# Optimization experiments

Hardware: AMD Instinct MI355X
Metric: run time of the kernel (lower is better)

Reference implementation:

```python
import jax, jax.numpy as jnp
import numpy as np

N_NODES = 50000
N_EDGES = 800000
D_IN = 128
D_OUT = 128
D_RED = 32  # out_features // reduction
ORDER = 3


def setup_inputs() -> dict:
    key = jax.random.key(0)
    ks = jax.random.split(key, 16)
    s = 1.0 / np.sqrt(D_IN)
    inp = {
        'features': jax.random.normal(ks[0], (N_NODES, D_IN), jnp.float32),
        'edge_row': jax.random.randint(ks[1], (N_EDGES,), 0, N_NODES, jnp.int32),
        'edge_col': jax.random.randint(ks[2], (N_EDGES,), 0, N_NODES, jnp.int32),
        'edge_val': jax.random.uniform(ks[3], (N_EDGES,), jnp.float32) / 16.0,  # ~1/avg_degree normalization
        'w1': jax.random.normal(ks[4], (D_IN, D_OUT), jnp.float32) * s,
        'b1': jax.random.normal(ks[5], (D_OUT,), jnp.float32) * s,
        'w2': jax.random.normal(ks[6], (D_IN, D_OUT), jnp.float32) * s,
        'b2': jax.random.normal(ks[7], (D_OUT,), jnp.float32) * s,
        'w3': jax.random.normal(ks[8], (D_IN, D_OUT), jnp.float32) * s,
        'b3': jax.random.normal(ks[9], (D_OUT,), jnp.float32) * s,
        'fc1_w': jax.random.normal(ks[10], (D_OUT, D_RED), jnp.float32) * s,
        'fc1_b': jax.random.normal(ks[11], (D_RED,), jnp.float32) * s,
        'fc2_w': jax.random.normal(ks[12], (D_RED, D_OUT), jnp.float32) * (1.0 / np.sqrt(D_RED)),
        'fc2_b': jax.random.normal(ks[13], (D_OUT,), jnp.float32) * s,
    }
    return inp


def reference(features, edge_row, edge_col, edge_val, w1, b1, w2, b2, w3, b3,
              fc1_w, fc1_b, fc2_w, fc2_b):
    def spmm(x):  # sparse [N,N] @ dense [N,D] via gather + segment_sum
        msgs = edge_val[:, None] * x[edge_col]          # [E, D]
        return jax.ops.segment_sum(msgs, edge_row, num_segments=N_NODES)

    def ngnn(w, b, order):
        h = jnp.tanh(features @ w)                      # active=True path
        for _ in range(order):                          # order spmm hops
            h = spmm(h)
        return h + b

    abstract = [ngnn(w, b, k + 1) for k, (w, b) in enumerate([(w1, b1), (w2, b2), (w3, b3)])]
    feats = jnp.stack(abstract, axis=0)                 # [order, N, D]
    m = jnp.mean(feats, axis=1)                         # [order, D]
    a = jax.nn.relu(m @ fc1_w + fc1_b) @ fc2_w + fc2_b  # [order, D]
    a = jax.nn.softmax(a, axis=0)                       # softmax over order dim
    out = jnp.einsum('ond,od->nd', feats, a)            # weighted combine
    return out
```

## Files before the change

### kernel.cpp

```cpp
#include <hip/hip_runtime.h>
#include <cstdint>

#define N_NODES 50000
#define N_EDGES 800000
#define EPCAP 64

typedef _Float16 half8 __attribute__((ext_vector_type(8)));
typedef float f32x4 __attribute__((ext_vector_type(4)));


__device__ inline unsigned pack_half2(float lo, float hi) {
    union { _Float16 h[2]; unsigned u; } cv;
    cv.h[0] = (_Float16)lo; cv.h[1] = (_Float16)hi;
    return cv.u;
}
__device__ inline float h_lo(unsigned u) {
    union { unsigned u; _Float16 h[2]; } cv; cv.u = u; return (float)cv.h[0];
}
__device__ inline float h_hi(unsigned u) {
    union { unsigned u; _Float16 h[2]; } cv; cv.u = u; return (float)cv.h[1];
}


__global__ __launch_bounds__(256) void pre_kernel(const int* __restrict__ rows,
                                                  const int* __restrict__ cols,
                                                  const float* __restrict__ vals,
                                                  int* __restrict__ cnt,
                                                  unsigned* __restrict__ ep,
                                                  const float* __restrict__ F,
                                                  const float* __restrict__ w3,
                                                  const float* __restrict__ w2,
                                                  const float* __restrict__ w1,
                                                  unsigned* __restrict__ T1) {
    __shared__ _Float16 Ws[128 * 128];
    int bx = blockIdx.x;
    int tid = threadIdx.x;

    if (bx >= 782) {
        int e = (bx - 782) * 256 + tid;
        int r = rows[e];
        int p = atomicAdd(&cnt[r], 1);
        union { _Float16 h; unsigned short s; } cv; cv.h = (_Float16)vals[e];
        if (p < EPCAP)
            __builtin_nontemporal_store(((unsigned)cv.s << 16) | (unsigned)cols[e],
                                        &ep[(size_t)r * EPCAP + p]);
        return;
    }

    int lane = tid & 63, wv = tid >> 6;
    int c = lane & 15, g = lane >> 4;
    int rowbase = bx * 64;

    half8 afr[4];
    {
        int row = rowbase + wv * 16 + c;
        if (row >= N_NODES) row = N_NODES - 1;
        const float* fr = F + (size_t)row * 128;
        #pragma unroll
        for (int ks = 0; ks < 4; ++ks) {
            const float4* s4 = (const float4*)(fr + ks * 32 + g * 8);
            float4 x0 = s4[0], x1 = s4[1];
            half8 a;
            a[0] = (_Float16)x0.x; a[1] = (_Float16)x0.y;
            a[2] = (_Float16)x0.z; a[3] = (_Float16)x0.w;
            a[4] = (_Float16)x1.x; a[5] = (_Float16)x1.y;
            a[6] = (_Float16)x1.z; a[7] = (_Float16)x1.w;
            afr[ks] = a;
        }
    }

    for (int b = 0; b < 3; ++b) {
        const float* W = (b == 0) ? w3 : (b == 1) ? w2 : w1;
        for (int i = tid; i < 16384; i += 256) {
            int d = i >> 7, j = i & 127;
            *(_Float16*)((char*)Ws + (((j * 128 + d) * 2) ^ ((j & 15) << 4))) = (_Float16)W[i];
        }
        __syncthreads();

        f32x4 zero = {0.f, 0.f, 0.f, 0.f};
        f32x4 acc[8];
        #pragma unroll
        for (int t = 0; t < 8; ++t) acc[t] = zero;

        #pragma unroll
        for (int ks = 0; ks < 4; ++ks) {
            #pragma unroll
            for (int t = 0; t < 8; ++t) {
                int j = t * 16 + c;
                int off = ((j * 128 + ks * 32 + g * 8) * 2) ^ ((j & 15) << 4);
                half8 bfr = *(const half8*)((const char*)Ws + off);
                acc[t] = __builtin_amdgcn_mfma_f32_16x16x32_f16(afr[ks], bfr, acc[t], 0, 0, 0);
            }
        }

        #pragma unroll
        for (int t = 0; t < 4; ++t) {
            int j = t * 16 + c;
            #pragma unroll
            for (int r = 0; r < 4; ++r) {
                int row = rowbase + wv * 16 + g * 4 + r;
                if (row < N_NODES)
                    T1[(size_t)row * 192 + b * 64 + j] =
                        pack_half2(tanhf(acc[t][r]), tanhf(acc[t + 4][r]));
            }
        }
        __syncthreads();
    }
}


template <int NCHUNK>
__global__ __launch_bounds__(512) void spmm_stage_kernel(const int* __restrict__ cnts,
                                                         const unsigned* __restrict__ ep,
                                                         const unsigned* __restrict__ x,
                                                         unsigned* __restrict__ ob0,
                                                         unsigned* __restrict__ obf,
                                                         float* __restrict__ csumK) {
    __shared__ float cs[128];
    int tid = threadIdx.x;
    if (tid < 128) cs[tid] = 0.f;
    __syncthreads();

    int row = blockIdx.x * 8 + (tid >> 6);
    int lane = tid & 63;
    int n = __builtin_amdgcn_readfirstlane(cnts[row]);
    n = n < EPCAP ? n : EPCAP;
    const unsigned* e0 = ep + (size_t)row * EPCAP;

    float ax[NCHUNK], ay[NCHUNK];
    #pragma unroll
    for (int cc = 0; cc < NCHUNK; ++cc) { ax[cc] = 0.f; ay[cc] = 0.f; }

    const unsigned* xl = x + lane;
    constexpr int U = 8;
    int i = 0;
    for (; i + U <= n; i += U) {
        unsigned p[U];
        #pragma unroll
        for (int u = 0; u < U; ++u) p[u] = e0[i + u];
        unsigned gx[U][NCHUNK];
        #pragma unroll
        for (int u = 0; u < U; ++u) {
            unsigned b = (p[u] & 0xFFFFu) * (unsigned)(NCHUNK * 64);
            #pragma unroll
            for (int cc = 0; cc < NCHUNK; ++cc) gx[u][cc] = xl[b + cc * 64];
        }
        #pragma unroll
        for (int u = 0; u < U; ++u) {
            union { unsigned short s; _Float16 h; } cu; cu.s = (unsigned short)(p[u] >> 16);
            float v = (float)cu.h;
            #pragma unroll
            for (int cc = 0; cc < NCHUNK; ++cc) {
                ax[cc] += v * h_lo(gx[u][cc]);
                ay[cc] += v * h_hi(gx[u][cc]);
            }
        }
    }
    for (; i < n; ++i) {
        unsigned p = e0[i];
        unsigned b = (p & 0xFFFFu) * (unsigned)(NCHUNK * 64);
        union { unsigned short s; _Float16 h; } cu; cu.s = (unsigned short)(p >> 16);
        float v = (float)cu.h;
        #pragma unroll
        for (int cc = 0; cc < NCHUNK; ++cc) {
            unsigned gg = xl[b + cc * 64];
            ax[cc] += v * h_lo(gg);
            ay[cc] += v * h_hi(gg);
        }
    }

    #pragma unroll
    for (int cc = 0; cc < NCHUNK - 1; ++cc)
        ob0[(size_t)row * ((NCHUNK - 1) * 64) + cc * 64 + lane] = pack_half2(ax[cc], ay[cc]);

    float fx = ax[NCHUNK - 1], fy = ay[NCHUNK - 1];
    obf[(size_t)row * 64 + lane] = pack_half2(fx, fy);
    atomicAdd(&cs[2 * lane + 0], fx);
    atomicAdd(&cs[2 * lane + 1], fy);
    __syncthreads();
    if (tid < 128) atomicAdd(&csumK[(blockIdx.x & 7) * 384 + tid], cs[tid]);
}


__global__ __launch_bounds__(256) void combine_kernel(float* __restrict__ out,
                                                      const unsigned* __restrict__ f1,
                                                      const unsigned* __restrict__ f2,
                                                      const unsigned* __restrict__ f3,
                                                      const float* __restrict__ csum,
                                                      const float* __restrict__ b1,
                                                      const float* __restrict__ b2,
                                                      const float* __restrict__ b3,
                                                      const float* __restrict__ fc1w,
                                                      const float* __restrict__ fc1b,
                                                      const float* __restrict__ fc2w,
                                                      const float* __restrict__ fc2b) {
    __shared__ float m[3][128];
    __shared__ float rr[3][32];
    __shared__ float wgt[3][128];
    int t = threadIdx.x;

    if (t < 128) {
        const float inv = 1.0f / (float)N_NODES;
        int slot = (t < 64) ? (2 * t) : (2 * (t - 64) + 1);
        #pragma unroll
        for (int k = 0; k < 3; ++k) {
            float s = 0.f;
            #pragma unroll
            for (int rep = 0; rep < 8; ++rep) s += csum[rep * 384 + k * 128 + slot];
            const float* bk = (k == 0) ? b1 : (k == 1) ? b2 : b3;
            m[k][t] = s * inv + bk[t];
        }
    }
    __syncthreads();
    if (t < 96) {
        int k = t >> 5, j = t & 31;
        float acc = fc1b[j];
        for (int d = 0; d < 128; ++d) acc += m[k][d] * fc1w[d * 32 + j];
        rr[k][j] = fmaxf(acc, 0.f);
    }
    __syncthreads();
    if (t < 128) {
        float a[3];
        #pragma unroll
        for (int k = 0; k < 3; ++k) {
            float acc = fc2b[t];
            for (int j = 0; j < 32; ++j) acc += rr[k][j] * fc2w[j * 128 + t];
            a[k] = acc;
        }
        float mx = fmaxf(a[0], fmaxf(a[1], a[2]));
        float e0 = expf(a[0] - mx), e1 = expf(a[1] - mx), e2 = expf(a[2] - mx);
        float s = e0 + e1 + e2;
        wgt[0][t] = e0 / s;
        wgt[1][t] = e1 / s;
        wgt[2][t] = e2 / s;
    }
    __syncthreads();

    const int total = N_NODES * 32;
    int idx0 = blockIdx.x * blockDim.x + threadIdx.x;
    int stride = gridDim.x * blockDim.x;
    int qb = idx0 & 31;
    float4 W0 = *(const float4*)&wgt[0][qb * 4];
    float4 W1 = *(const float4*)&wgt[1][qb * 4];
    float4 W2 = *(const float4*)&wgt[2][qb * 4];
    float4 B1 = ((const float4*)b1)[qb];
    float4 B2 = ((const float4*)b2)[qb];
    float4 B3 = ((const float4*)b3)[qb];
    bool hi = qb >= 16;
    int qm = qb & 15;
    for (int idx = idx0; idx < total; idx += stride) {
        int row = idx >> 5;
        uint4 u1 = ((const uint4*)f1)[row * 16 + qm];
        uint4 u2 = ((const uint4*)f2)[row * 16 + qm];
        uint4 u3 = ((const uint4*)f3)[row * 16 + qm];
        float f1x = hi ? h_hi(u1.x) : h_lo(u1.x);
        float f1y = hi ? h_hi(u1.y) : h_lo(u1.y);
        float f1z = hi ? h_hi(u1.z) : h_lo(u1.z);
        float f1w = hi ? h_hi(u1.w) : h_lo(u1.w);
        float f2x = hi ? h_hi(u2.x) : h_lo(u2.x);
        float f2y = hi ? h_hi(u2.y) : h_lo(u2.y);
        float f2z = hi ? h_hi(u2.z) : h_lo(u2.z);
        float f2w = hi ? h_hi(u2.w) : h_lo(u2.w);
        float f3x = hi ? h_hi(u3.x) : h_lo(u3.x);
        float f3y = hi ? h_hi(u3.y) : h_lo(u3.y);
        float f3z = hi ? h_hi(u3.z) : h_lo(u3.z);
        float f3w = hi ? h_hi(u3.w) : h_lo(u3.w);
        float4 o;
        o.x = (f1x + B1.x) * W0.x + (f2x + B2.x) * W1.x + (f3x + B3.x) * W2.x;
        o.y = (f1y + B1.y) * W0.y + (f2y + B2.y) * W1.y + (f3y + B3.y) * W2.y;
        o.z = (f1z + B1.z) * W0.z + (f2z + B2.z) * W1.z + (f3z + B3.z) * W2.z;
        o.w = (f1w + B1.w) * W0.w + (f2w + B2.w) * W1.w + (f3w + B3.w) * W2.w;
        ((float4*)out)[idx] = o;
    }
}


extern "C" void kernel_launch(void* const* d_in, const int* in_sizes, int n_in,
                              void* d_out, int out_size, void* d_ws, size_t ws_size,
                              hipStream_t stream) {
    const float* F    = (const float*)d_in[0];
    const int*   erow = (const int*)d_in[1];
    const int*   ecol = (const int*)d_in[2];
    const float* eval_ = (const float*)d_in[3];
    const float* w1 = (const float*)d_in[4];  const float* b1 = (const float*)d_in[5];
    const float* w2 = (const float*)d_in[6];  const float* b2 = (const float*)d_in[7];
    const float* w3 = (const float*)d_in[8];  const float* b3 = (const float*)d_in[9];
    const float* fc1w = (const float*)d_in[10]; const float* fc1b = (const float*)d_in[11];
    const float* fc2w = (const float*)d_in[12]; const float* fc2b = (const float*)d_in[13];
    float* out = (float*)d_out;

    char* ws = (char*)d_ws;
    size_t off = 0;
    auto alloc = [&](size_t bytes) -> void* {
        off = (off + 255) & ~(size_t)255;
        void* p = ws + off;
        off += bytes;
        return p;
    };
    unsigned* T1   = (unsigned*)alloc((size_t)N_NODES * 192 * 4);
    unsigned* T2   = (unsigned*)alloc((size_t)N_NODES * 128 * 4);
    unsigned* T3   = (unsigned*)alloc((size_t)N_NODES * 64 * 4);
    unsigned* f1h  = (unsigned*)alloc((size_t)N_NODES * 64 * 4);
    unsigned* ep   = (unsigned*)alloc((size_t)N_NODES * EPCAP * 4);
    int*   counts  = (int*)alloc((size_t)N_NODES * sizeof(int));
    float* csum    = (float*)alloc(8 * 3 * 128 * sizeof(float));
    unsigned* f2h  = T1;
    unsigned* f3h  = T1 + (size_t)N_NODES * 64;

    size_t zlen = (size_t)((char*)csum + 8 * 3 * 128 * sizeof(float) - (char*)counts);
    hipMemsetAsync(counts, 0, zlen, stream);

    pre_kernel<<<782 + 3125, 256, 0, stream>>>(erow, ecol, eval_, counts, ep,
                                               F, w3, w2, w1, T1);

    const int spmmGrid = N_NODES / 8;

    spmm_stage_kernel<3><<<spmmGrid, 512, 0, stream>>>(counts, ep, T1, T2, f1h, csum + 0 * 128);
    spmm_stage_kernel<2><<<spmmGrid, 512, 0, stream>>>(counts, ep, T2, T3, f2h, csum + 1 * 128);
    spmm_stage_kernel<1><<<spmmGrid, 512, 0, stream>>>(counts, ep, T3, nullptr, f3h, csum + 2 * 128);

    combine_kernel<<<2048, 256, 0, stream>>>(out, f1h, f2h, f3h, csum, b1, b2, b3,
                                             fc1w, fc1b, fc2w, fc2b);
}
```

Measured before the change: 345.6 us.

## Precompute attention weights via transposed-vector dots and fuse combine into Horner SpMM passes

Computes per-order feature means algebraically as dot products of H_k with s_k = (A^T)^k 1, obtained from cheap scalar scatter passes, so the softmax weights are known before the wide SpMMs. The weighted combine is then folded into a nested Horner-style sequence of three SpMM passes that each gather only 64-word half2 rows. This reduces gather bandwidth relative to the earlier 3/2/1-chunk stages and removes the separate combine read pass. In exchange it adds atomic scatter kernels, a reduction kernel and a tiny serial fc kernel, and changes fp16 rounding order.

```diff
diff --git a/kernel.cpp b/kernel.cpp
--- a/kernel.cpp
+++ b/kernel.cpp
@@ -27,11 +27,14 @@
                                                   const float* __restrict__ vals,
                                                   int* __restrict__ cnt,
                                                   unsigned* __restrict__ ep,
+                                                  float* __restrict__ qsum,
                                                   const float* __restrict__ F,
                                                   const float* __restrict__ w3,
                                                   const float* __restrict__ w2,
                                                   const float* __restrict__ w1,
-                                                  unsigned* __restrict__ T1) {
+                                                  unsigned* __restrict__ H3,
+                                                  unsigned* __restrict__ H2,
+                                                  unsigned* __restrict__ H1) {
     __shared__ _Float16 Ws[128 * 128];
     int bx = blockIdx.x;
     int tid = threadIdx.x;
@@ -39,11 +42,14 @@
     if (bx >= 782) {
         int e = (bx - 782) * 256 + tid;
         int r = rows[e];
+        int c = cols[e];
+        float vf = vals[e];
         int p = atomicAdd(&cnt[r], 1);
-        union { _Float16 h; unsigned short s; } cv; cv.h = (_Float16)vals[e];
+        union { _Float16 h; unsigned short s; } cv; cv.h = (_Float16)vf;
         if (p < EPCAP)
-            __builtin_nontemporal_store(((unsigned)cv.s << 16) | (unsigned)cols[e],
+            __builtin_nontemporal_store(((unsigned)cv.s << 16) | (unsigned)c,
                                         &ep[(size_t)r * EPCAP + p]);
+        atomicAdd(&qsum[c], vf);
         return;
     }
 
@@ -71,6 +77,7 @@
 
     for (int b = 0; b < 3; ++b) {
         const float* W = (b == 0) ? w3 : (b == 1) ? w2 : w1;
+        unsigned* Hb   = (b == 0) ? H3 : (b == 1) ? H2 : H1;
         for (int i = tid; i < 16384; i += 256) {
             int d = i >> 7, j = i & 127;
             *(_Float16*)((char*)Ws + (((j * 128 + d) * 2) ^ ((j & 15) << 4))) = (_Float16)W[i];
@@ -100,7 +107,7 @@
             for (int r = 0; r < 4; ++r) {
                 int row = rowbase + wv * 16 + g * 4 + r;
                 if (row < N_NODES)
-                    T1[(size_t)row * 192 + b * 64 + j] =
+                    Hb[(size_t)row * 64 + j] =
                         pack_half2(tanhf(acc[t][r]), tanhf(acc[t + 4][r]));
             }
         }
@@ -109,107 +116,66 @@
 }
 
 
-template <int NCHUNK>
-__global__ __launch_bounds__(512) void spmm_stage_kernel(const int* __restrict__ cnts,
-                                                         const unsigned* __restrict__ ep,
-                                                         const unsigned* __restrict__ x,
-                                                         unsigned* __restrict__ ob0,
-                                                         unsigned* __restrict__ obf,
-                                                         float* __restrict__ csumK) {
+__global__ __launch_bounds__(256) void svec_kernel(const int* __restrict__ rows,
+                                                   const int* __restrict__ cols,
+                                                   const float* __restrict__ vals,
+                                                   const float* __restrict__ sin_,
+                                                   float* __restrict__ sout) {
+    int e = blockIdx.x * 256 + threadIdx.x;
+    atomicAdd(&sout[cols[e]], vals[e] * sin_[rows[e]]);
+}
+
+
+__global__ __launch_bounds__(256) void dots_kernel(const float* __restrict__ s1,
+                                                   const float* __restrict__ s2,
+                                                   const float* __restrict__ s3,
+                                                   const unsigned* __restrict__ H1,
+                                                   const unsigned* __restrict__ H2,
+                                                   const unsigned* __restrict__ H3,
+                                                   float* __restrict__ ddot) {
+    int k = blockIdx.y;
+    const float* sv = (k == 0) ? s1 : (k == 1) ? s2 : s3;
+    const unsigned* H = (k == 0) ? H1 : (k == 1) ? H2 : H3;
     __shared__ float cs[128];
-    int tid = threadIdx.x;
+    int tid = threadIdx.x, lane = tid & 63, w = tid >> 6;
     if (tid < 128) cs[tid] = 0.f;
     __syncthreads();
-
-    int row = blockIdx.x * 8 + (tid >> 6);
-    int lane = tid & 63;
-    int n = __builtin_amdgcn_readfirstlane(cnts[row]);
-    n = n < EPCAP ? n : EPCAP;
-    const unsigned* e0 = ep + (size_t)row * EPCAP;
-
-    float ax[NCHUNK], ay[NCHUNK];
-    #pragma unroll
-    for (int cc = 0; cc < NCHUNK; ++cc) { ax[cc] = 0.f; ay[cc] = 0.f; }
-
-    const unsigned* xl = x + lane;
-    constexpr int U = 8;
-    int i = 0;
-    for (; i + U <= n; i += U) {
-        unsigned p[U];
-        #pragma unroll
-        for (int u = 0; u < U; ++u) p[u] = e0[i + u];
-        unsigned gx[U][NCHUNK];
-        #pragma unroll
-        for (int u = 0; u < U; ++u) {
-            unsigned b = (p[u] & 0xFFFFu) * (unsigned)(NCHUNK * 64);
-            #pragma unroll
-            for (int cc = 0; cc < NCHUNK; ++cc) gx[u][cc] = xl[b + cc * 64];
-        }
-        #pragma unroll
-        for (int u = 0; u < U; ++u) {
-            union { unsigned short s; _Float16 h; } cu; cu.s = (unsigned short)(p[u] >> 16);
-            float v = (float)cu.h;
-            #pragma unroll
-            for (int cc = 0; cc < NCHUNK; ++cc) {
-                ax[cc] += v * h_lo(gx[u][cc]);
-                ay[cc] += v * h_hi(gx[u][cc]);
-            }
-        }
-    }
-    for (; i < n; ++i) {
-        unsigned p = e0[i];
-        unsigned b = (p & 0xFFFFu) * (unsigned)(NCHUNK * 64);
-        union { unsigned short s; _Float16 h; } cu; cu.s = (unsigned short)(p >> 16);
-        float v = (float)cu.h;
-        #pragma unroll
-        for (int cc = 0; cc < NCHUNK; ++cc) {
-            unsigned gg = xl[b + cc * 64];
-            ax[cc] += v * h_lo(gg);
-            ay[cc] += v * h_hi(gg);
-        }
-    }
-
-    #pragma unroll
-    for (int cc = 0; cc < NCHUNK - 1; ++cc)
-        ob0[(size_t)row * ((NCHUNK - 1) * 64) + cc * 64 + lane] = pack_half2(ax[cc], ay[cc]);
-
-    float fx = ax[NCHUNK - 1], fy = ay[NCHUNK - 1];
-    obf[(size_t)row * 64 + lane] = pack_half2(fx, fy);
-    atomicAdd(&cs[2 * lane + 0], fx);
-    atomicAdd(&cs[2 * lane + 1], fy);
+    float aLo = 0.f, aHi = 0.f;
+    for (int r = blockIdx.x * 4 + w; r < N_NODES; r += 256 * 4) {
+        float v = sv[r];
+        unsigned u = H[(size_t)r * 64 + lane];
+        aLo += v * h_lo(u);
+        aHi += v * h_hi(u);
+    }
+    atomicAdd(&cs[2 * lane + 0], aLo);
+    atomicAdd(&cs[2 * lane + 1], aHi);
     __syncthreads();
-    if (tid < 128) atomicAdd(&csumK[(blockIdx.x & 7) * 384 + tid], cs[tid]);
-}
-
-
-__global__ __launch_bounds__(256) void combine_kernel(float* __restrict__ out,
-                                                      const unsigned* __restrict__ f1,
-                                                      const unsigned* __restrict__ f2,
-                                                      const unsigned* __restrict__ f3,
-                                                      const float* __restrict__ csum,
-                                                      const float* __restrict__ b1,
-                                                      const float* __restrict__ b2,
-                                                      const float* __restrict__ b3,
-                                                      const float* __restrict__ fc1w,
-                                                      const float* __restrict__ fc1b,
-                                                      const float* __restrict__ fc2w,
-                                                      const float* __restrict__ fc2b) {
+    if (tid < 128) atomicAdd(&ddot[(blockIdx.x & 7) * 384 + k * 128 + tid], cs[tid]);
+}
+
+
+__global__ __launch_bounds__(128) void fc_alpha_kernel(const float* __restrict__ ddot,
+                                                       const float* __restrict__ b1,
+                                                       const float* __restrict__ b2,
+                                                       const float* __restrict__ b3,
+                                                       const float* __restrict__ fc1w,
+                                                       const float* __restrict__ fc1b,
+                                                       const float* __restrict__ fc2w,
+                                                       const float* __restrict__ fc2b,
+                                                       float* __restrict__ wgt,
+                                                       float* __restrict__ cb) {
     __shared__ float m[3][128];
     __shared__ float rr[3][32];
-    __shared__ float wgt[3][128];
     int t = threadIdx.x;
-
-    if (t < 128) {
-        const float inv = 1.0f / (float)N_NODES;
-        int slot = (t < 64) ? (2 * t) : (2 * (t - 64) + 1);
-        #pragma unroll
-        for (int k = 0; k < 3; ++k) {
-            float s = 0.f;
-            #pragma unroll
-            for (int rep = 0; rep < 8; ++rep) s += csum[rep * 384 + k * 128 + slot];
-            const float* bk = (k == 0) ? b1 : (k == 1) ? b2 : b3;
-            m[k][t] = s * inv + bk[t];
-        }
+    const float inv = 1.0f / (float)N_NODES;
+    int slot = (t < 64) ? (2 * t) : (2 * (t - 64) + 1);
+    #pragma unroll
+    for (int k = 0; k < 3; ++k) {
+        float s = 0.f;
+        #pragma unroll
+        for (int rep = 0; rep < 8; ++rep) s += ddot[rep * 384 + k * 128 + slot];
+        const float* bk = (k == 0) ? b1 : (k == 1) ? b2 : b3;
+        m[k][t] = s * inv + bk[t];
     }
     __syncthreads();
     if (t < 96) {
@@ -219,58 +185,83 @@
         rr[k][j] = fmaxf(acc, 0.f);
     }
     __syncthreads();
-    if (t < 128) {
-        float a[3];
-        #pragma unroll
-        for (int k = 0; k < 3; ++k) {
-            float acc = fc2b[t];
-            for (int j = 0; j < 32; ++j) acc += rr[k][j] * fc2w[j * 128 + t];
-            a[k] = acc;
-        }
-        float mx = fmaxf(a[0], fmaxf(a[1], a[2]));
-        float e0 = expf(a[0] - mx), e1 = expf(a[1] - mx), e2 = expf(a[2] - mx);
-        float s = e0 + e1 + e2;
-        wgt[0][t] = e0 / s;
-        wgt[1][t] = e1 / s;
-        wgt[2][t] = e2 / s;
-    }
-    __syncthreads();
-
-    const int total = N_NODES * 32;
-    int idx0 = blockIdx.x * blockDim.x + threadIdx.x;
-    int stride = gridDim.x * blockDim.x;
-    int qb = idx0 & 31;
-    float4 W0 = *(const float4*)&wgt[0][qb * 4];
-    float4 W1 = *(const float4*)&wgt[1][qb * 4];
-    float4 W2 = *(const float4*)&wgt[2][qb * 4];
-    float4 B1 = ((const float4*)b1)[qb];
-    float4 B2 = ((const float4*)b2)[qb];
-    float4 B3 = ((const float4*)b3)[qb];
-    bool hi = qb >= 16;
-    int qm = qb & 15;
-    for (int idx = idx0; idx < total; idx += stride) {
-        int row = idx >> 5;
-        uint4 u1 = ((const uint4*)f1)[row * 16 + qm];
-        uint4 u2 = ((const uint4*)f2)[row * 16 + qm];
-        uint4 u3 = ((const uint4*)f3)[row * 16 + qm];
-        float f1x = hi ? h_hi(u1.x) : h_lo(u1.x);
-        float f1y = hi ? h_hi(u1.y) : h_lo(u1.y);
-        float f1z = hi ? h_hi(u1.z) : h_lo(u1.z);
-        float f1w = hi ? h_hi(u1.w) : h_lo(u1.w);
-        float f2x = hi ? h_hi(u2.x) : h_lo(u2.x);
-        float f2y = hi ? h_hi(u2.y) : h_lo(u2.y);
-        float f2z = hi ? h_hi(u2.z) : h_lo(u2.z);
-        float f2w = hi ? h_hi(u2.w) : h_lo(u2.w);
-        float f3x = hi ? h_hi(u3.x) : h_lo(u3.x);
-        float f3y = hi ? h_hi(u3.y) : h_lo(u3.y);
-        float f3z = hi ? h_hi(u3.z) : h_lo(u3.z);
-        float f3w = hi ? h_hi(u3.w) : h_lo(u3.w);
-        float4 o;
-        o.x = (f1x + B1.x) * W0.x + (f2x + B2.x) * W1.x + (f3x + B3.x) * W2.x;
-        o.y = (f1y + B1.y) * W0.y + (f2y + B2.y) * W1.y + (f3y + B3.y) * W2.y;
-        o.z = (f1z + B1.z) * W0.z + (f2z + B2.z) * W1.z + (f3z + B3.z) * W2.z;
-        o.w = (f1w + B1.w) * W0.w + (f2w + B2.w) * W1.w + (f3w + B3.w) * W2.w;
-        ((float4*)out)[idx] = o;
+    float a[3];
+    #pragma unroll
+    for (int k = 0; k < 3; ++k) {
+        float acc = fc2b[t];
+        for (int j = 0; j < 32; ++j) acc += rr[k][j] * fc2w[j * 128 + t];
+        a[k] = acc;
+    }
+    float mx = fmaxf(a[0], fmaxf(a[1], a[2]));
+    float e0 = expf(a[0] - mx), e1 = expf(a[1] - mx), e2 = expf(a[2] - mx);
+    float s = e0 + e1 + e2;
+    float g0 = e0 / s, g1 = e1 / s, g2 = e2 / s;
+    wgt[0 * 128 + t] = g0;
+    wgt[1 * 128 + t] = g1;
+    wgt[2 * 128 + t] = g2;
+    cb[t] = g0 * b1[t] + g1 * b2[t] + g2 * b3[t];
+}
+
+
+template <int MODE>
+__global__ __launch_bounds__(512) void pass_kernel(const int* __restrict__ cnts,
+                                                   const unsigned* __restrict__ ep,
+                                                   const unsigned* __restrict__ x,
+                                                   const unsigned* __restrict__ hstream,
+                                                   const float* __restrict__ sG,
+                                                   const float* __restrict__ sS,
+                                                   const float* __restrict__ cb,
+                                                   unsigned* __restrict__ outH,
+                                                   float* __restrict__ outF) {
+    int tid = threadIdx.x;
+    int row = blockIdx.x * 8 + (tid >> 6);
+    int lane = tid & 63;
+    int n = __builtin_amdgcn_readfirstlane(cnts[row]);
+    n = n < EPCAP ? n : EPCAP;
+    const unsigned* e0 = ep + (size_t)row * EPCAP;
+    const unsigned* xl = x + lane;
+
+    float fx = 0.f, fy = 0.f;
+    constexpr int U = 8;
+    int i = 0;
+    for (; i + U <= n; i += U) {
+        unsigned p[U];
+        #pragma unroll
+        for (int u = 0; u < U; ++u) p[u] = e0[i + u];
+        unsigned gg[U];
+        #pragma unroll
+        for (int u = 0; u < U; ++u) gg[u] = xl[(p[u] & 0xFFFFu) * 64u];
+        #pragma unroll
+        for (int u = 0; u < U; ++u) {
+            union { unsigned short s; _Float16 h; } cu; cu.s = (unsigned short)(p[u] >> 16);
+            float v = (float)cu.h;
+            fx += v * h_lo(gg[u]);
+            fy += v * h_hi(gg[u]);
+        }
+    }
+    for (; i < n; ++i) {
+        unsigned p = e0[i];
+        unsigned gg = xl[(p & 0xFFFFu) * 64u];
+        union { unsigned short s; _Float16 h; } cu; cu.s = (unsigned short)(p >> 16);
+        float v = (float)cu.h;
+        fx += v * h_lo(gg);
+        fy += v * h_hi(gg);
+    }
+
+    if constexpr (MODE == 3) {
+        unsigned hs = hstream[(size_t)row * 64 + lane];
+        float gLo = sG[lane], gHi = sG[lane + 64];
+        float tLo = sS[lane], tHi = sS[lane + 64];
+        outH[(size_t)row * 64 + lane] =
+            pack_half2(tLo * h_lo(hs) + gLo * fx, tHi * h_hi(hs) + gHi * fy);
+    } else if constexpr (MODE == 2) {
+        unsigned hs = hstream[(size_t)row * 64 + lane];
+        float tLo = sS[lane], tHi = sS[lane + 64];
+        outH[(size_t)row * 64 + lane] =
+            pack_half2(tLo * h_lo(hs) + fx, tHi * h_hi(hs) + fy);
+    } else {
+        outF[(size_t)row * 128 + lane] = fx + cb[lane];
+        outF[(size_t)row * 128 + 64 + lane] = fy + cb[lane + 64];
     }
 }
 
@@ -297,28 +288,40 @@
         off += bytes;
         return p;
     };
-    unsigned* T1   = (unsigned*)alloc((size_t)N_NODES * 192 * 4);
-    unsigned* T2   = (unsigned*)alloc((size_t)N_NODES * 128 * 4);
-    unsigned* T3   = (unsigned*)alloc((size_t)N_NODES * 64 * 4);
-    unsigned* f1h  = (unsigned*)alloc((size_t)N_NODES * 64 * 4);
-    unsigned* ep   = (unsigned*)alloc((size_t)N_NODES * EPCAP * 4);
-    int*   counts  = (int*)alloc((size_t)N_NODES * sizeof(int));
-    float* csum    = (float*)alloc(8 * 3 * 128 * sizeof(float));
-    unsigned* f2h  = T1;
-    unsigned* f3h  = T1 + (size_t)N_NODES * 64;
-
-    size_t zlen = (size_t)((char*)csum + 8 * 3 * 128 * sizeof(float) - (char*)counts);
+    const size_t tabBytes = (size_t)N_NODES * 64 * 4;
+    unsigned* H3 = (unsigned*)alloc(tabBytes);
+    unsigned* H2 = (unsigned*)alloc(tabBytes);
+    unsigned* H1 = (unsigned*)alloc(tabBytes);
+    unsigned* Y2 = (unsigned*)alloc(tabBytes);
+    unsigned* Y1 = (unsigned*)alloc(tabBytes);
+    unsigned* ep = (unsigned*)alloc((size_t)N_NODES * EPCAP * 4);
+    int*   counts = (int*)alloc((size_t)N_NODES * sizeof(int));
+    float* qsum   = (float*)alloc((size_t)N_NODES * sizeof(float));
+    float* s2     = (float*)alloc((size_t)N_NODES * sizeof(float));
+    float* s3     = (float*)alloc((size_t)N_NODES * sizeof(float));
+    float* ddot   = (float*)alloc(8 * 3 * 128 * sizeof(float));
+    float* wgt    = (float*)alloc(3 * 128 * sizeof(float));
+    float* cb     = (float*)alloc(128 * sizeof(float));
+
+    size_t zlen = (size_t)((char*)ddot + 8 * 3 * 128 * sizeof(float) - (char*)counts);
     hipMemsetAsync(counts, 0, zlen, stream);
 
-    pre_kernel<<<782 + 3125, 256, 0, stream>>>(erow, ecol, eval_, counts, ep,
-                                               F, w3, w2, w1, T1);
-
-    const int spmmGrid = N_NODES / 8;
-
-    spmm_stage_kernel<3><<<spmmGrid, 512, 0, stream>>>(counts, ep, T1, T2, f1h, csum + 0 * 128);
-    spmm_stage_kernel<2><<<spmmGrid, 512, 0, stream>>>(counts, ep, T2, T3, f2h, csum + 1 * 128);
-    spmm_stage_kernel<1><<<spmmGrid, 512, 0, stream>>>(counts, ep, T3, nullptr, f3h, csum + 2 * 128);
-
-    combine_kernel<<<2048, 256, 0, stream>>>(out, f1h, f2h, f3h, csum, b1, b2, b3,
-                                             fc1w, fc1b, fc2w, fc2b);
-}
+    pre_kernel<<<782 + 3125, 256, 0, stream>>>(erow, ecol, eval_, counts, ep, qsum,
+                                               F, w3, w2, w1, H3, H2, H1);
+
+    svec_kernel<<<3125, 256, 0, stream>>>(erow, ecol, eval_, qsum, s2);
+    svec_kernel<<<3125, 256, 0, stream>>>(erow, ecol, eval_, s2, s3);
+
+    dots_kernel<<<dim3(256, 3), 256, 0, stream>>>(qsum, s2, s3, H1, H2, H3, ddot);
+
+    fc_alpha_kernel<<<1, 128, 0, stream>>>(ddot, b1, b2, b3, fc1w, fc1b, fc2w, fc2b, wgt, cb);
+
+    const int passGrid = N_NODES / 8;
+
+    pass_kernel<3><<<passGrid, 512, 0, stream>>>(counts, ep, H3, H2,
+                                                 wgt + 2 * 128, wgt + 1 * 128, nullptr, Y2, nullptr);
+    pass_kernel<2><<<passGrid, 512, 0, stream>>>(counts, ep, Y2, H1,
+                                                 nullptr, wgt + 0 * 128, nullptr, Y1, nullptr);
+    pass_kernel<1><<<passGrid, 512, 0, stream>>>(counts, ep, Y1, nullptr,
+                                                 nullptr, nullptr, cb, nullptr, out);
+}
```

New measurement: 354.1 us. +2.5%, slower.
